# Kernel tuning notes

Measured on AMD Instinct MI355X. Metric: run time of the kernel, lower is better.

The kernel has to match this reference:

```python
import jax, jax.numpy as jnp
import numpy as np

EPS = 1e-5  # torch LayerNorm default
NUM_HEADS = 12


def layer_norm(x, g, b):
    m = jnp.mean(x, axis=-1, keepdims=True)
    v = jnp.var(x, axis=-1, keepdims=True)
    return (x - m) * jax.lax.rsqrt(v + EPS) * g + b


def split_heads(x):
    B, N, C = x.shape
    return x.reshape(B, N, NUM_HEADS, C // NUM_HEADS).transpose(0, 2, 1, 3)  # [B,H,N,D]


def merge_heads(x):
    B, H, N, D = x.shape
    return x.transpose(0, 2, 1, 3).reshape(B, N, H * D)


def attn_core(q, k, v, mask):
    # q:[B,H,Nq,D], k/v:[B,H,Nk,D], mask:[B,Nk] float (1=keep)
    d = q.shape[-1]
    scores = jnp.einsum('bhqd,bhkd->bhqk', q, k) * (d ** -0.5)
    scores = scores + (1.0 - mask)[:, None, None, :] * -5.0
    a = jax.nn.softmax(scores, axis=-1)
    return jnp.einsum('bhqk,bhkd->bhqd', a, v)


def setup_inputs() -> dict:
    key = jax.random.key(0)
    B, N, C = 4, 1024, 768
    Hd = C * 4  # mlp hidden = 3072
    ks = jax.random.split(key, 12)
    s = 0.02
    inp = {
        'x': jax.random.normal(ks[0], (B, N, C), jnp.float32),
        'encoder_out': jax.random.normal(ks[1], (B, N, C), jnp.float32),
        'mask': jnp.ones((B, N), jnp.float32),
        'encoder_mask': jnp.ones((B, N), jnp.float32),
        'ln1_g': jnp.ones((C,), jnp.float32), 'ln1_b': jnp.zeros((C,), jnp.float32),
        'qkv_w': jax.random.normal(ks[2], (C, 3 * C), jnp.float32) * s,
        'sa_proj_w': jax.random.normal(ks[3], (C, C), jnp.float32) * s,
        'sa_proj_b': jnp.zeros((C,), jnp.float32),
        'ln2_g': jnp.ones((C,), jnp.float32), 'ln2_b': jnp.zeros((C,), jnp.float32),
        'q_w': jax.random.normal(ks[4], (C, C), jnp.float32) * s,
        'kv_w': jax.random.normal(ks[5], (C, 2 * C), jnp.float32) * s,
        'ca_proj_w': jax.random.normal(ks[6], (C, C), jnp.float32) * s,
        'ca_proj_b': jnp.zeros((C,), jnp.float32),
        'ln3_g': jnp.ones((C,), jnp.float32), 'ln3_b': jnp.zeros((C,), jnp.float32),
        'fc1_w': jax.random.normal(ks[7], (C, Hd), jnp.float32) * s,
        'fc1_b': jnp.zeros((Hd,), jnp.float32),
        'fc2_w': jax.random.normal(ks[8], (Hd, C), jnp.float32) * s,
        'fc2_b': jnp.zeros((C,), jnp.float32),
    }
    return inp


def reference(x, encoder_out, mask, encoder_mask,
              ln1_g, ln1_b, qkv_w, sa_proj_w, sa_proj_b,
              ln2_g, ln2_b, q_w, kv_w, ca_proj_w, ca_proj_b,
              ln3_g, ln3_b, fc1_w, fc1_b, fc2_w, fc2_b):
    B, N, C = x.shape
    D = C // NUM_HEADS
    # --- self attention ---
    h = layer_norm(x, ln1_g, ln1_b)
    qkv = (h @ qkv_w).reshape(B, N, 3, NUM_HEADS, D)
    q = qkv[:, :, 0].transpose(0, 2, 1, 3)
    k = qkv[:, :, 1].transpose(0, 2, 1, 3)
    v = qkv[:, :, 2].transpose(0, 2, 1, 3)
    o = merge_heads(attn_core(q, k, v, mask)) @ sa_proj_w + sa_proj_b
    x = x + o
    # --- cross attention ---
    h = layer_norm(x, ln2_g, ln2_b)
    q = split_heads(h @ q_w)
    Be, Ne, Ce = encoder_out.shape
    kv = (encoder_out @ kv_w).reshape(Be, Ne, 2, NUM_HEADS, D)
    k = kv[:, :, 0].transpose(0, 2, 1, 3)
    v = kv[:, :, 1].transpose(0, 2, 1, 3)
    o = merge_heads(attn_core(q, k, v, encoder_mask)) @ ca_proj_w + ca_proj_b
    x = x + o
    # --- MLP (exact GELU, like torch nn.GELU default) ---
    h = layer_norm(x, ln3_g, ln3_b)
    h = jax.nn.gelu(h @ fc1_w + fc1_b, approximate=False) @ fc2_w + fc2_b
    return x + h
```

## Files before the change

### kernel.cpp

```cpp
#include <hip/hip_runtime.h>

typedef __attribute__((ext_vector_type(8))) __bf16 bf16x8;
typedef __attribute__((ext_vector_type(4))) float f32x4;

__device__ __forceinline__ void gload_lds16(const __bf16* g, __bf16* l) {
    __builtin_amdgcn_global_load_lds(
        (const __attribute__((address_space(1))) void*)g,
        (__attribute__((address_space(3))) void*)l,
        16, 0, 0);
}

__global__ void transpose_f2b(const float* __restrict__ in, __bf16* __restrict__ outp,
                              int R, int Ccols) {
    __shared__ __bf16 tile[32][33];
    int bx = blockIdx.x * 32, by = blockIdx.y * 32;
    int tx = threadIdx.x & 31, ty = threadIdx.x >> 5;
#pragma unroll
    for (int i = ty; i < 32; i += 8)
        tile[i][tx] = (__bf16)in[(size_t)(by + i) * Ccols + bx + tx];
    __syncthreads();
#pragma unroll
    for (int i = ty; i < 32; i += 8)
        outp[(size_t)(bx + i) * R + by + tx] = tile[tx][i];
}

__global__ void cvt_f2b(const float* __restrict__ in, __bf16* __restrict__ outp) {
    int i = blockIdx.x * blockDim.x + threadIdx.x;
    float4 v = ((const float4*)in)[i];
    __bf16 o4[4] = {(__bf16)v.x, (__bf16)v.y, (__bf16)v.z, (__bf16)v.w};
    *(uint2*)(outp + (size_t)i * 4) = *(const uint2*)o4;
}

__global__ __launch_bounds__(256) void ln_kernel(const float* __restrict__ x,
                                                 const float* __restrict__ g,
                                                 const float* __restrict__ b,
                                                 __bf16* __restrict__ o) {
    int row = blockIdx.x, tid = threadIdx.x;
    const float* xr = x + (size_t)row * 768;
    float v0 = xr[tid], v1 = xr[tid + 256], v2 = xr[tid + 512];
    float s = v0 + v1 + v2, s2 = v0 * v0 + v1 * v1 + v2 * v2;
#pragma unroll
    for (int d = 32; d >= 1; d >>= 1) {
        s += __shfl_xor(s, d);
        s2 += __shfl_xor(s2, d);
    }
    __shared__ float red[8];
    int wave = tid >> 6, lane = tid & 63;
    if (!lane) { red[wave] = s; red[4 + wave] = s2; }
    __syncthreads();
    s = red[0] + red[1] + red[2] + red[3];
    s2 = red[4] + red[5] + red[6] + red[7];
    float mean = s * (1.0f / 768.0f);
    float var = s2 * (1.0f / 768.0f) - mean * mean;
    float inv = rsqrtf(var + 1e-5f);
    o[(size_t)row * 768 + tid]       = (__bf16)((v0 - mean) * inv * g[tid]       + b[tid]);
    o[(size_t)row * 768 + tid + 256] = (__bf16)((v1 - mean) * inv * g[tid + 256] + b[tid + 256]);
    o[(size_t)row * 768 + tid + 512] = (__bf16)((v2 - mean) * inv * g[tid + 512] + b[tid + 512]);
}

template <int BIAS, int RESID, int GELU, typename TO>
__global__ __launch_bounds__(256, 2) void gemm_nt(
    const __bf16* __restrict__ A, int lda,
    const __bf16* __restrict__ Bt, int ldb,
    TO* __restrict__ C, int ldc,
    const float* __restrict__ bias,
    const float* __restrict__ resid,
    int K) {
    __shared__ __bf16 lA[128 * 32];
    __shared__ __bf16 lB[128 * 32];
    const int tid = threadIdx.x;
    const int wave = tid >> 6, lane = tid & 63;
    const int wm = wave >> 1, wn = wave & 1;
    const int bn = blockIdx.x * 128, bm = blockIdx.y * 128;
    const int ln15 = lane & 15, hi = lane >> 4;

    f32x4 acc[4][4] = {};

    const int srow = tid >> 2;
    const int scol = (((tid & 3) ^ (srow & 3)) * 8);
    const __bf16* gA0 = A + (size_t)(bm + srow) * lda + scol;
    const __bf16* gA1 = A + (size_t)(bm + 64 + srow) * lda + scol;
    const __bf16* gB0 = Bt + (size_t)(bn + srow) * ldb + scol;
    const __bf16* gB1 = Bt + (size_t)(bn + 64 + srow) * ldb + scol;
    __bf16* lA0 = lA + wave * 512;
    __bf16* lA1 = lA + 2048 + wave * 512;
    __bf16* lB0 = lB + wave * 512;
    __bf16* lB1 = lB + 2048 + wave * 512;

    const int rswz = (hi * 8) ^ ((lane & 3) * 8);
    const __bf16* rA = lA + (wm * 64 + ln15) * 32 + rswz;
    const __bf16* rB = lB + (wn * 64 + ln15) * 32 + rswz;

    for (int k0 = 0; k0 < K; k0 += 32) {
        gload_lds16(gA0 + k0, lA0);
        gload_lds16(gA1 + k0, lA1);
        gload_lds16(gB0 + k0, lB0);
        gload_lds16(gB1 + k0, lB1);
        __syncthreads();
        bf16x8 af[4], bf[4];
#pragma unroll
        for (int m = 0; m < 4; ++m) af[m] = *(const bf16x8*)(rA + m * 512);
#pragma unroll
        for (int n = 0; n < 4; ++n) bf[n] = *(const bf16x8*)(rB + n * 512);
#pragma unroll
        for (int m = 0; m < 4; ++m)
#pragma unroll
            for (int n = 0; n < 4; ++n)
                acc[m][n] = __builtin_amdgcn_mfma_f32_16x16x32_bf16(af[m], bf[n], acc[m][n], 0, 0, 0);
        __syncthreads();
    }

#pragma unroll
    for (int m = 0; m < 4; ++m)
#pragma unroll
        for (int n = 0; n < 4; ++n)
#pragma unroll
            for (int r = 0; r < 4; ++r) {
                int row = bm + wm * 64 + m * 16 + hi * 4 + r;
                int col = bn + wn * 64 + n * 16 + ln15;
                float v = acc[m][n][r];
                if (BIAS) v += bias[col];
                if (GELU) v = 0.5f * v * (1.0f + erff(v * 0.70710678118f));
                if (RESID) v += resid[(size_t)row * ldc + col];
                C[(size_t)row * ldc + col] = (TO)v;
            }
}

__global__ __launch_bounds__(256, 2) void attn_kernel(
    const __bf16* __restrict__ Qp, int ldq, int qcol,
    const __bf16* __restrict__ Kp, int ldk, int kcol,
    const __bf16* __restrict__ Vp, int ldv, int vcol,
    const float* __restrict__ mask,
    __bf16* __restrict__ Out) {
    __shared__ __bf16 lK[64 * 64];
    __shared__ __bf16 lV[64 * 64];
    __shared__ __bf16 lP[4][16 * 64];
    const int tid = threadIdx.x, wave = tid >> 6, lane = tid & 63;
    const int bh = blockIdx.y, b = bh / 12, h = bh % 12;
    const int qt = blockIdx.x;
    const int ln15 = lane & 15, hi = lane >> 4;

    const __bf16* qrow = Qp + (size_t)(b * 1024 + qt * 64 + wave * 16 + ln15) * ldq + qcol + h * 64;
    bf16x8 qf0 = *(const bf16x8*)(qrow + hi * 8);
    bf16x8 qf1 = *(const bf16x8*)(qrow + 32 + hi * 8);

    float m_run[4] = {-1e30f, -1e30f, -1e30f, -1e30f};
    float l_run[4] = {0.f, 0.f, 0.f, 0.f};
    f32x4 oacc[4] = {};

    const int skey = tid >> 3;
    const int ssrc = (((tid & 7) ^ (skey & 7)) * 8);
    const __bf16* gK = Kp + (size_t)(b * 1024 + skey) * ldk + kcol + h * 64 + ssrc;
    __bf16* lK0 = lK + wave * 512;
    __bf16* lK1 = lK + 2048 + wave * 512;

    const int vkey = tid & 63;
    const int vdb = wave * 16;
    const __bf16* gV = Vp + (size_t)(b * 1024 + vkey) * ldv + vcol + h * 64 + vdb;

    const int kswz = (lane & 7) * 8;
    const __bf16* rK = lK + ln15 * 64;
    const __bf16* rV = lV + ln15 * 64;
    __bf16* wP = lP[wave];
    const __bf16* rP = lP[wave] + ln15 * 64;

    for (int kt = 0; kt < 16; ++kt) {
        const size_t tb = (size_t)kt * 64;
        gload_lds16(gK + tb * ldk, lK0);
        gload_lds16(gK + (tb + 32) * ldk, lK1);
        bf16x8 v0 = *(const bf16x8*)(gV + tb * ldv);
        bf16x8 v1 = *(const bf16x8*)(gV + tb * ldv + 8);
#pragma unroll
        for (int j = 0; j < 8; ++j) {
            lV[(vdb + j) * 64 + (vkey ^ (j * 8))] = v0[j];
            lV[(vdb + 8 + j) * 64 + (vkey ^ (j * 8))] = v1[j];
        }
        __syncthreads();

        f32x4 s[4];
#pragma unroll
        for (int n = 0; n < 4; ++n) {
            bf16x8 kf0 = *(const bf16x8*)(rK + n * 1024 + ((hi * 8) ^ kswz));
            bf16x8 kf1 = *(const bf16x8*)(rK + n * 1024 + ((hi * 8 + 32) ^ kswz));
            f32x4 z = {};
            z = __builtin_amdgcn_mfma_f32_16x16x32_bf16(qf0, kf0, z, 0, 0, 0);
            s[n] = __builtin_amdgcn_mfma_f32_16x16x32_bf16(qf1, kf1, z, 0, 0, 0);
        }
        float mb[4];
#pragma unroll
        for (int n = 0; n < 4; ++n)
            mb[n] = (1.0f - mask[b * 1024 + kt * 64 + n * 16 + ln15]) * -5.0f;
#pragma unroll
        for (int n = 0; n < 4; ++n)
#pragma unroll
            for (int r = 0; r < 4; ++r)
                s[n][r] = s[n][r] * 0.125f + mb[n];

        float sc[4];
#pragma unroll
        for (int r = 0; r < 4; ++r) {
            float mx = fmaxf(fmaxf(s[0][r], s[1][r]), fmaxf(s[2][r], s[3][r]));
#pragma unroll
            for (int d = 1; d < 16; d <<= 1) mx = fmaxf(mx, __shfl_xor(mx, d));
            float mn = fmaxf(m_run[r], mx);
            sc[r] = __expf(m_run[r] - mn);
            m_run[r] = mn;
            float ls = 0.f;
#pragma unroll
            for (int n = 0; n < 4; ++n) {
                s[n][r] = __expf(s[n][r] - mn);
                ls += s[n][r];
            }
#pragma unroll
            for (int d = 1; d < 16; d <<= 1) ls += __shfl_xor(ls, d);
            l_run[r] = l_run[r] * sc[r] + ls;
        }
#pragma unroll
        for (int n = 0; n < 4; ++n)
#pragma unroll
            for (int r = 0; r < 4; ++r)
                oacc[n][r] *= sc[r];

#pragma unroll
        for (int n = 0; n < 4; ++n)
#pragma unroll
            for (int r = 0; r < 4; ++r) {
                int prow = hi * 4 + r;
                wP[prow * 64 + ((n * 16 + ln15) ^ ((prow & 7) * 8))] = (__bf16)s[n][r];
            }
        bf16x8 pf0 = *(const bf16x8*)(rP + ((hi * 8) ^ kswz));
        bf16x8 pf1 = *(const bf16x8*)(rP + ((hi * 8 + 32) ^ kswz));
#pragma unroll
        for (int n = 0; n < 4; ++n) {
            bf16x8 vf0 = *(const bf16x8*)(rV + n * 1024 + ((hi * 8) ^ kswz));
            bf16x8 vf1 = *(const bf16x8*)(rV + n * 1024 + ((hi * 8 + 32) ^ kswz));
            oacc[n] = __builtin_amdgcn_mfma_f32_16x16x32_bf16(pf0, vf0, oacc[n], 0, 0, 0);
            oacc[n] = __builtin_amdgcn_mfma_f32_16x16x32_bf16(pf1, vf1, oacc[n], 0, 0, 0);
        }
        __syncthreads();
    }

#pragma unroll
    for (int n = 0; n < 4; ++n)
#pragma unroll
        for (int r = 0; r < 4; ++r) {
            int row = b * 1024 + qt * 64 + wave * 16 + hi * 4 + r;
            int col = h * 64 + n * 16 + ln15;
            Out[(size_t)row * 768 + col] = (__bf16)(oacc[n][r] / l_run[r]);
        }
}

extern "C" void kernel_launch(void* const* d_in, const int* in_sizes, int n_in,
                              void* d_out, int out_size, void* d_ws, size_t ws_size,
                              hipStream_t stream) {
    const float* x     = (const float*)d_in[0];
    const float* enc   = (const float*)d_in[1];
    const float* mask  = (const float*)d_in[2];
    const float* emask = (const float*)d_in[3];
    const float* ln1_g = (const float*)d_in[4];
    const float* ln1_b = (const float*)d_in[5];
    const float* qkv_w = (const float*)d_in[6];
    const float* sa_w  = (const float*)d_in[7];
    const float* sa_b  = (const float*)d_in[8];
    const float* ln2_g = (const float*)d_in[9];
    const float* ln2_b = (const float*)d_in[10];
    const float* q_w   = (const float*)d_in[11];
    const float* kv_w  = (const float*)d_in[12];
    const float* ca_w  = (const float*)d_in[13];
    const float* ca_b  = (const float*)d_in[14];
    const float* ln3_g = (const float*)d_in[15];
    const float* ln3_b = (const float*)d_in[16];
    const float* fc1_w = (const float*)d_in[17];
    const float* fc1_b = (const float*)d_in[18];
    const float* fc2_w = (const float*)d_in[19];
    const float* fc2_b = (const float*)d_in[20];
    float* out = (float*)d_out;

    char* w = (char*)d_ws;
    size_t off = 0;
    auto alloc = [&](size_t bytes) { void* p = w + off; off += bytes; return p; };
    __bf16* qkv_t = (__bf16*)alloc((size_t)2304 * 768 * 2);
    __bf16* sa_t  = (__bf16*)alloc((size_t)768 * 768 * 2);
    __bf16* q_t   = (__bf16*)alloc((size_t)768 * 768 * 2);
    __bf16* kv_t  = (__bf16*)alloc((size_t)1536 * 768 * 2);
    __bf16* ca_t  = (__bf16*)alloc((size_t)768 * 768 * 2);
    __bf16* fc1_t = (__bf16*)alloc((size_t)3072 * 768 * 2);
    __bf16* fc2_t = (__bf16*)alloc((size_t)768 * 3072 * 2);
    __bf16* H     = (__bf16*)alloc((size_t)4096 * 768 * 2);
    __bf16* QKV   = (__bf16*)alloc((size_t)4096 * 2304 * 2);
    __bf16* ATT   = (__bf16*)alloc((size_t)4096 * 768 * 2);
    float*  X1    = (float*)alloc((size_t)4096 * 768 * 4);
    float*  X2    = (float*)alloc((size_t)4096 * 768 * 4);
    __bf16* encb  = (__bf16*)alloc((size_t)4096 * 768 * 2);
    __bf16* HID   = QKV;
    __bf16* Qb    = QKV;
    __bf16* KVb   = QKV + (size_t)4096 * 768;

    dim3 blk(256);
    transpose_f2b<<<dim3(72, 24), blk, 0, stream>>>(qkv_w, qkv_t, 768, 2304);
    transpose_f2b<<<dim3(24, 24), blk, 0, stream>>>(sa_w, sa_t, 768, 768);
    transpose_f2b<<<dim3(24, 24), blk, 0, stream>>>(q_w, q_t, 768, 768);
    transpose_f2b<<<dim3(48, 24), blk, 0, stream>>>(kv_w, kv_t, 768, 1536);
    transpose_f2b<<<dim3(24, 24), blk, 0, stream>>>(ca_w, ca_t, 768, 768);
    transpose_f2b<<<dim3(96, 24), blk, 0, stream>>>(fc1_w, fc1_t, 768, 3072);
    transpose_f2b<<<dim3(24, 96), blk, 0, stream>>>(fc2_w, fc2_t, 3072, 768);
    cvt_f2b<<<dim3(3072), blk, 0, stream>>>(enc, encb);

    ln_kernel<<<4096, blk, 0, stream>>>(x, ln1_g, ln1_b, H);
    gemm_nt<0, 0, 0, __bf16><<<dim3(18, 32), blk, 0, stream>>>(H, 768, qkv_t, 768, QKV, 2304, nullptr, nullptr, 768);
    attn_kernel<<<dim3(16, 48), blk, 0, stream>>>(QKV, 2304, 0, QKV, 2304, 768, QKV, 2304, 1536, mask, ATT);
    gemm_nt<1, 1, 0, float><<<dim3(6, 32), blk, 0, stream>>>(ATT, 768, sa_t, 768, X1, 768, sa_b, x, 768);
    ln_kernel<<<4096, blk, 0, stream>>>(X1, ln2_g, ln2_b, H);
    gemm_nt<0, 0, 0, __bf16><<<dim3(6, 32), blk, 0, stream>>>(H, 768, q_t, 768, Qb, 768, nullptr, nullptr, 768);
    gemm_nt<0, 0, 0, __bf16><<<dim3(12, 32), blk, 0, stream>>>(encb, 768, kv_t, 768, KVb, 1536, nullptr, nullptr, 768);
    attn_kernel<<<dim3(16, 48), blk, 0, stream>>>(Qb, 768, 0, KVb, 1536, 0, KVb, 1536, 768, emask, ATT);
    gemm_nt<1, 1, 0, float><<<dim3(6, 32), blk, 0, stream>>>(ATT, 768, ca_t, 768, X2, 768, ca_b, X1, 768);
    ln_kernel<<<4096, blk, 0, stream>>>(X2, ln3_g, ln3_b, H);
    gemm_nt<1, 0, 1, __bf16><<<dim3(24, 32), blk, 0, stream>>>(H, 768, fc1_t, 768, HID, 3072, fc1_b, nullptr, 768);
    gemm_nt<1, 1, 0, float><<<dim3(6, 32), blk, 0, stream>>>(HID, 3072, fc2_t, 3072, out, 768, fc2_b, X2, 3072);
}
```

Measured before the change: 485.3 us.

## Double-buffer GEMM LDS loads, add 64-row tiles, lazy softmax rescale

The GEMM kernel now double-buffers its LDS tiles. It issues the next K-slice's global-to-LDS loads before computing the current one, with explicit vmcnt waits and barriers, so load latency can overlap with MFMA work. A BM=64 tile variant is added and used for the N=768 projections (sa/q/ca/fc2), doubling their grid to improve CU occupancy. The attention kernel's online softmax now rescales the accumulator only when the running max grows by more than 8, which skips most exp and multiply work. This relies on exp values staying bounded under a stale max. LDS use doubles, and the manual waitcnt counts must exactly match the number of loads issued.

```diff
diff --git a/kernel.cpp b/kernel.cpp
--- a/kernel.cpp
+++ b/kernel.cpp
@@ -58,7 +58,7 @@
     o[(size_t)row * 768 + tid + 512] = (__bf16)((v2 - mean) * inv * g[tid + 512] + b[tid + 512]);
 }
 
-template <int BIAS, int RESID, int GELU, typename TO>
+template <int BM, int BIAS, int RESID, int GELU, typename TO>
 __global__ __launch_bounds__(256, 2) void gemm_nt(
     const __bf16* __restrict__ A, int lda,
     const __bf16* __restrict__ Bt, int ldb,
@@ -66,15 +66,18 @@
     const float* __restrict__ bias,
     const float* __restrict__ resid,
     int K) {
-    __shared__ __bf16 lA[128 * 32];
-    __shared__ __bf16 lB[128 * 32];
+    __shared__ __bf16 lA[2][BM * 32];
+    __shared__ __bf16 lB[2][128 * 32];
+    constexpr int WCOLS = 256 / BM;
+    constexpr int NF = (BM == 128) ? 4 : 2;
+    constexpr int WNSP = (BM == 128) ? 64 : 32;
     const int tid = threadIdx.x;
     const int wave = tid >> 6, lane = tid & 63;
-    const int wm = wave >> 1, wn = wave & 1;
-    const int bn = blockIdx.x * 128, bm = blockIdx.y * 128;
+    const int wm = wave / WCOLS, wn = wave % WCOLS;
+    const int bn = blockIdx.x * 128, bm = blockIdx.y * BM;
     const int ln15 = lane & 15, hi = lane >> 4;
 
-    f32x4 acc[4][4] = {};
+    f32x4 acc[4][NF] = {};
 
     const int srow = tid >> 2;
     const int scol = (((tid & 3) ^ (srow & 3)) * 8);
@@ -82,42 +85,58 @@
     const __bf16* gA1 = A + (size_t)(bm + 64 + srow) * lda + scol;
     const __bf16* gB0 = Bt + (size_t)(bn + srow) * ldb + scol;
     const __bf16* gB1 = Bt + (size_t)(bn + 64 + srow) * ldb + scol;
-    __bf16* lA0 = lA + wave * 512;
-    __bf16* lA1 = lA + 2048 + wave * 512;
-    __bf16* lB0 = lB + wave * 512;
-    __bf16* lB1 = lB + 2048 + wave * 512;
 
     const int rswz = (hi * 8) ^ ((lane & 3) * 8);
-    const __bf16* rA = lA + (wm * 64 + ln15) * 32 + rswz;
-    const __bf16* rB = lB + (wn * 64 + ln15) * 32 + rswz;
-
-    for (int k0 = 0; k0 < K; k0 += 32) {
-        gload_lds16(gA0 + k0, lA0);
-        gload_lds16(gA1 + k0, lA1);
-        gload_lds16(gB0 + k0, lB0);
-        gload_lds16(gB1 + k0, lB1);
-        __syncthreads();
-        bf16x8 af[4], bf[4];
+    const int rAoff = (wm * 64 + ln15) * 32 + rswz;
+    const int rBoff = (wn * WNSP + ln15) * 32 + rswz;
+
+    auto STAGE = [&](int buf, int k0) {
+        gload_lds16(gA0 + k0, lA[buf] + wave * 512);
+        if constexpr (BM == 128) gload_lds16(gA1 + k0, lA[buf] + 2048 + wave * 512);
+        gload_lds16(gB0 + k0, lB[buf] + wave * 512);
+        gload_lds16(gB1 + k0, lB[buf] + 2048 + wave * 512);
+    };
+    auto COMPUTE = [&](int buf) {
+        const __bf16* rA = lA[buf] + rAoff;
+        const __bf16* rB = lB[buf] + rBoff;
+        bf16x8 af[4], bfr[NF];
 #pragma unroll
         for (int m = 0; m < 4; ++m) af[m] = *(const bf16x8*)(rA + m * 512);
 #pragma unroll
-        for (int n = 0; n < 4; ++n) bf[n] = *(const bf16x8*)(rB + n * 512);
+        for (int n = 0; n < NF; ++n) bfr[n] = *(const bf16x8*)(rB + n * 512);
 #pragma unroll
         for (int m = 0; m < 4; ++m)
 #pragma unroll
-            for (int n = 0; n < 4; ++n)
-                acc[m][n] = __builtin_amdgcn_mfma_f32_16x16x32_bf16(af[m], bf[n], acc[m][n], 0, 0, 0);
-        __syncthreads();
+            for (int n = 0; n < NF; ++n)
+                acc[m][n] = __builtin_amdgcn_mfma_f32_16x16x32_bf16(af[m], bfr[n], acc[m][n], 0, 0, 0);
+    };
+
+    const int nt = K >> 5;
+    STAGE(0, 0);
+    for (int t = 0; t < nt - 1; ++t) {
+        const int cur = t & 1;
+        STAGE(cur ^ 1, (t + 1) << 5);
+        if constexpr (BM == 128) asm volatile("s_waitcnt vmcnt(4)" ::: "memory");
+        else                     asm volatile("s_waitcnt vmcnt(3)" ::: "memory");
+        __builtin_amdgcn_s_barrier();
+        __builtin_amdgcn_sched_barrier(0);
+        COMPUTE(cur);
+        __builtin_amdgcn_sched_barrier(0);
+        __builtin_amdgcn_s_barrier();
     }
+    asm volatile("s_waitcnt vmcnt(0)" ::: "memory");
+    __builtin_amdgcn_s_barrier();
+    __builtin_amdgcn_sched_barrier(0);
+    COMPUTE((nt - 1) & 1);
 
 #pragma unroll
     for (int m = 0; m < 4; ++m)
 #pragma unroll
-        for (int n = 0; n < 4; ++n)
+        for (int n = 0; n < NF; ++n)
 #pragma unroll
             for (int r = 0; r < 4; ++r) {
                 int row = bm + wm * 64 + m * 16 + hi * 4 + r;
-                int col = bn + wn * 64 + n * 16 + ln15;
+                int col = bn + wn * WNSP + n * 16 + ln15;
                 float v = acc[m][n][r];
                 if (BIAS) v += bias[col];
                 if (GELU) v = 0.5f * v * (1.0f + erff(v * 0.70710678118f));
@@ -196,30 +215,28 @@
             for (int r = 0; r < 4; ++r)
                 s[n][r] = s[n][r] * 0.125f + mb[n];
 
-        float sc[4];
 #pragma unroll
         for (int r = 0; r < 4; ++r) {
             float mx = fmaxf(fmaxf(s[0][r], s[1][r]), fmaxf(s[2][r], s[3][r]));
 #pragma unroll
             for (int d = 1; d < 16; d <<= 1) mx = fmaxf(mx, __shfl_xor(mx, d));
-            float mn = fmaxf(m_run[r], mx);
-            sc[r] = __expf(m_run[r] - mn);
-            m_run[r] = mn;
+            if (mx > m_run[r] + 8.f) {
+                float scf = __expf(m_run[r] - mx);
+                m_run[r] = mx;
+                l_run[r] *= scf;
+#pragma unroll
+                for (int n = 0; n < 4; ++n) oacc[n][r] *= scf;
+            }
             float ls = 0.f;
 #pragma unroll
             for (int n = 0; n < 4; ++n) {
-                s[n][r] = __expf(s[n][r] - mn);
+                s[n][r] = __expf(s[n][r] - m_run[r]);
                 ls += s[n][r];
             }
 #pragma unroll
             for (int d = 1; d < 16; d <<= 1) ls += __shfl_xor(ls, d);
-            l_run[r] = l_run[r] * sc[r] + ls;
-        }
-#pragma unroll
-        for (int n = 0; n < 4; ++n)
-#pragma unroll
-            for (int r = 0; r < 4; ++r)
-                oacc[n][r] *= sc[r];
+            l_run[r] += ls;
+        }
 
 #pragma unroll
         for (int n = 0; n < 4; ++n)
@@ -307,15 +324,15 @@
     cvt_f2b<<<dim3(3072), blk, 0, stream>>>(enc, encb);
 
     ln_kernel<<<4096, blk, 0, stream>>>(x, ln1_g, ln1_b, H);
-    gemm_nt<0, 0, 0, __bf16><<<dim3(18, 32), blk, 0, stream>>>(H, 768, qkv_t, 768, QKV, 2304, nullptr, nullptr, 768);
+    gemm_nt<128, 0, 0, 0, __bf16><<<dim3(18, 32), blk, 0, stream>>>(H, 768, qkv_t, 768, QKV, 2304, nullptr, nullptr, 768);
     attn_kernel<<<dim3(16, 48), blk, 0, stream>>>(QKV, 2304, 0, QKV, 2304, 768, QKV, 2304, 1536, mask, ATT);
-    gemm_nt<1, 1, 0, float><<<dim3(6, 32), blk, 0, stream>>>(ATT, 768, sa_t, 768, X1, 768, sa_b, x, 768);
+    gemm_nt<64, 1, 1, 0, float><<<dim3(6, 64), blk, 0, stream>>>(ATT, 768, sa_t, 768, X1, 768, sa_b, x, 768);
     ln_kernel<<<4096, blk, 0, stream>>>(X1, ln2_g, ln2_b, H);
-    gemm_nt<0, 0, 0, __bf16><<<dim3(6, 32), blk, 0, stream>>>(H, 768, q_t, 768, Qb, 768, nullptr, nullptr, 768);
-    gemm_nt<0, 0, 0, __bf16><<<dim3(12, 32), blk, 0, stream>>>(encb, 768, kv_t, 768, KVb, 1536, nullptr, nullptr, 768);
+    gemm_nt<64, 0, 0, 0, __bf16><<<dim3(6, 64), blk, 0, stream>>>(H, 768, q_t, 768, Qb, 768, nullptr, nullptr, 768);
+    gemm_nt<128, 0, 0, 0, __bf16><<<dim3(12, 32), blk, 0, stream>>>(encb, 768, kv_t, 768, KVb, 1536, nullptr, nullptr, 768);
     attn_kernel<<<dim3(16, 48), blk, 0, stream>>>(Qb, 768, 0, KVb, 1536, 0, KVb, 1536, 768, emask, ATT);
-    gemm_nt<1, 1, 0, float><<<dim3(6, 32), blk, 0, stream>>>(ATT, 768, ca_t, 768, X2, 768, ca_b, X1, 768);
+    gemm_nt<64, 1, 1, 0, float><<<dim3(6, 64), blk, 0, stream>>>(ATT, 768, ca_t, 768, X2, 768, ca_b, X1, 768);
     ln_kernel<<<4096, blk, 0, stream>>>(X2, ln3_g, ln3_b, H);
-    gemm_nt<1, 0, 1, __bf16><<<dim3(24, 32), blk, 0, stream>>>(H, 768, fc1_t, 768, HID, 3072, fc1_b, nullptr, 768);
-    gemm_nt<1, 1, 0, float><<<dim3(6, 32), blk, 0, stream>>>(HID, 3072, fc2_t, 3072, out, 768, fc2_b, X2, 3072);
-}
+    gemm_nt<128, 1, 0, 1, __bf16><<<dim3(24, 32), blk, 0, stream>>>(H, 768, fc1_t, 768, HID, 3072, fc1_b, nullptr, 768);
+    gemm_nt<64, 1, 1, 0, float><<<dim3(6, 64), blk, 0, stream>>>(HID, 3072, fc2_t, 3072, out, 768, fc2_b, X2, 3072);
+}
```

Measured after the change: 467.2 us. 1.04x faster.
